# Optimization experiments

Hardware: AMD Instinct MI355X
Metric: run time of the kernel (lower is better)

The kernel has to match this reference:

```python
import jax, jax.numpy as jnp
import numpy as np

N = 8192
IN_F = 256
OUT_F = 256


def setup_inputs() -> dict:
    key = jax.random.key(0)
    k_v, k_adj, k1, k2, k3, kb = jax.random.split(key, 6)
    stdv = 1.0 / np.sqrt(OUT_F)
    V = jax.random.normal(k_v, (N, IN_F), dtype=jnp.float32)
    adj = jax.random.randint(k_adj, (N, N), 0, 4, dtype=jnp.int32)
    w1 = jax.random.uniform(k1, (IN_F, OUT_F), jnp.float32, -stdv, stdv)
    w2 = jax.random.uniform(k2, (IN_F, OUT_F), jnp.float32, -stdv, stdv)
    w3 = jax.random.uniform(k3, (IN_F, OUT_F), jnp.float32, -stdv, stdv)
    bias = jax.random.uniform(kb, (OUT_F,), jnp.float32, -stdv, stdv)
    return {"V": V, "adj": adj, "w1": w1, "w2": w2, "w3": w3, "bias": bias}


def reference(V, adj, w1, w2, w3, bias):
    # typed relational GCN: for each edge type k in {1,2,3},
    # aggregate (adj==k) @ (V @ wk), then sum and add bias
    o1 = jnp.matmul((adj == 1).astype(jnp.float32), jnp.matmul(V, w1))
    o2 = jnp.matmul((adj == 2).astype(jnp.float32), jnp.matmul(V, w2))
    o3 = jnp.matmul((adj == 3).astype(jnp.float32), jnp.matmul(V, w3))
    return o1 + o2 + o3 + bias
```

## Files before the change

kernel.cpp:

```cpp
#include <hip/hip_runtime.h>

typedef __attribute__((ext_vector_type(4))) float f32x4;
typedef __attribute__((ext_vector_type(16))) float f32x16;
typedef __attribute__((ext_vector_type(4))) unsigned short u16x4;
typedef __attribute__((ext_vector_type(4))) int i32x4;
typedef __attribute__((ext_vector_type(8))) __bf16 bf16x8;

union FragAB {
  u16x4 u[2];
  i32x4 v;
  bf16x8 f;
};

static __device__ __forceinline__ unsigned short f2bf(float x) {
  union { float f; unsigned u; } v;
  v.f = x;
  unsigned r = v.u + 0x7FFFu + ((v.u >> 16) & 1u);
  return (unsigned short)(r >> 16);
}

#define NN 8192

__global__ __launch_bounds__(256) void k_bias(const float* __restrict__ bias,
                                              float* __restrict__ out) {
  out[(size_t)blockIdx.x * 256 + threadIdx.x] = bias[threadIdx.x];
}

__global__ __launch_bounds__(256) void k_transform(
    const float* __restrict__ V, const float* __restrict__ w1,
    const float* __restrict__ w2, const float* __restrict__ w3,
    unsigned short* __restrict__ Bp) {
  int bx = blockIdx.x;
  int rb = bx & 63;
  int nb = bx >> 6;
  int nc0 = (nb & 3) * 64;
  int tid = threadIdx.x;
  int lane = tid & 63;
  int wv = tid >> 6;
  int wm = wv >> 1, wn = wv & 1;
  int q = lane >> 4, l16 = lane & 15;

  __shared__ unsigned short tA[128][36];
  __shared__ unsigned short tB[64][36];

  f32x4 acc[4][2];
#pragma unroll
  for (int i = 0; i < 4; i++)
#pragma unroll
    for (int j = 0; j < 2; j++) acc[i][j] = (f32x4)0.0f;

  for (int kk = 0; kk < 256; kk += 32) {
    {
      int r = tid >> 1, c0 = (tid & 1) * 16;
      const float* src = V + (size_t)(rb * 128 + r) * 256 + kk + c0;
      f32x4 f0 = *(const f32x4*)(src + 0);
      f32x4 f1 = *(const f32x4*)(src + 4);
      f32x4 f2 = *(const f32x4*)(src + 8);
      f32x4 f3 = *(const f32x4*)(src + 12);
      unsigned short* d = &tA[r][c0];
      d[0] = f2bf(f0.x);  d[1] = f2bf(f0.y);  d[2] = f2bf(f0.z);  d[3] = f2bf(f0.w);
      d[4] = f2bf(f1.x);  d[5] = f2bf(f1.y);  d[6] = f2bf(f1.z);  d[7] = f2bf(f1.w);
      d[8] = f2bf(f2.x);  d[9] = f2bf(f2.y);  d[10] = f2bf(f2.z); d[11] = f2bf(f2.w);
      d[12] = f2bf(f3.x); d[13] = f2bf(f3.y); d[14] = f2bf(f3.z); d[15] = f2bf(f3.w);
    }
    {
      int r = tid >> 3, cg = (tid & 7) * 8;
      size_t off = (size_t)(kk + r) * 256 + nc0 + cg;
      f32x4 g0, g1;
      if (nb < 4) {
        g0 = *(const f32x4*)(w1 + off);
        g1 = *(const f32x4*)(w1 + off + 4);
      } else if (nb < 8) {
        g0 = *(const f32x4*)(w2 + off);
        g1 = *(const f32x4*)(w2 + off + 4);
      } else {
        f32x4 a0 = *(const f32x4*)(w1 + off), a1 = *(const f32x4*)(w1 + off + 4);
        f32x4 b0 = *(const f32x4*)(w2 + off), b1 = *(const f32x4*)(w2 + off + 4);
        f32x4 d0 = *(const f32x4*)(w3 + off), d1 = *(const f32x4*)(w3 + off + 4);
        g0 = d0 - a0 - b0;
        g1 = d1 - a1 - b1;
      }
      tB[cg + 0][r] = f2bf(g0.x); tB[cg + 1][r] = f2bf(g0.y);
      tB[cg + 2][r] = f2bf(g0.z); tB[cg + 3][r] = f2bf(g0.w);
      tB[cg + 4][r] = f2bf(g1.x); tB[cg + 5][r] = f2bf(g1.y);
      tB[cg + 6][r] = f2bf(g1.z); tB[cg + 7][r] = f2bf(g1.w);
    }
    __syncthreads();
    FragAB af[4], bf[2];
#pragma unroll
    for (int mt = 0; mt < 4; mt++) {
      const unsigned short* p = &tA[wm * 64 + mt * 16 + l16][q * 8];
      af[mt].u[0] = *(const u16x4*)p;
      af[mt].u[1] = *(const u16x4*)(p + 4);
    }
#pragma unroll
    for (int nt = 0; nt < 2; nt++) {
      const unsigned short* p = &tB[wn * 32 + nt * 16 + l16][q * 8];
      bf[nt].u[0] = *(const u16x4*)p;
      bf[nt].u[1] = *(const u16x4*)(p + 4);
    }
#pragma unroll
    for (int mt = 0; mt < 4; mt++)
#pragma unroll
      for (int nt = 0; nt < 2; nt++)
        acc[mt][nt] = __builtin_amdgcn_mfma_f32_16x16x32_bf16(
            af[mt].f, bf[nt].f, acc[mt][nt], 0, 0, 0);
    __syncthreads();
  }
  int ty = nb >> 2;
#pragma unroll
  for (int mt = 0; mt < 4; mt++)
#pragma unroll
    for (int nt = 0; nt < 2; nt++) {
      int n = (nb & 3) * 64 + wn * 32 + nt * 16 + l16;
      int j0 = rb * 128 + wm * 64 + mt * 16 + q * 4;
      u16x4 hv;
      hv.x = f2bf(acc[mt][nt].x);
      hv.y = f2bf(acc[mt][nt].y);
      hv.z = f2bf(acc[mt][nt].z);
      hv.w = f2bf(acc[mt][nt].w);
      size_t idx = (size_t)ty * 2097152 + (size_t)(j0 >> 4) * 4096 + n * 16 + (j0 & 15);
      *(u16x4*)(Bp + idx) = hv;
    }
}

__global__ __launch_bounds__(256) void k_pack(const int* __restrict__ adj,
                                              unsigned* __restrict__ P) {
  int bx = blockIdx.x;
  int rowblk = bx >> 3, ks = bx & 7;
  int t = threadIdx.x;
  int r0 = rowblk * 32;
  __shared__ unsigned hal[32][129];

  int rl = t >> 7;
  int o = t & 127;
  const int* src0 = adj + (size_t)(r0 + rl) * NN + ks * 1024 + o * 8;
  i32x4 v0 = *(const i32x4*)src0;
  i32x4 v1 = *(const i32x4*)(src0 + 4);
  for (int p = 0; p < 16; p++) {
    i32x4 u0 = v0, u1 = v1;
    if (p < 15) {
      const int* s = src0 + (size_t)(p + 1) * 2 * NN;
      v0 = *(const i32x4*)s;
      v1 = *(const i32x4*)(s + 4);
    }
    unsigned b = (unsigned)(u0.x & 3) | ((unsigned)(u0.y & 3) << 2) |
                 ((unsigned)(u0.z & 3) << 4) | ((unsigned)(u0.w & 3) << 6) |
                 ((unsigned)(u1.x & 3) << 8) | ((unsigned)(u1.y & 3) << 10) |
                 ((unsigned)(u1.z & 3) << 12) | ((unsigned)(u1.w & 3) << 14);
    hal[p * 2 + rl][o] = b;
  }
  __syncthreads();
  for (int i = 0; i < 8; i++) {
    int oi = i * 256 + t;
    int row = oi & 31, sq = oi >> 5;
    int s = sq >> 1, q = sq & 1;
    unsigned lo = hal[row][s * 4 + q];
    unsigned hi = hal[row][s * 4 + 2 + q];
    P[((size_t)(ks * 32 + s) * 2 + q) * 8192 + r0 + row] = lo | (hi << 16);
  }
}

static __device__ __forceinline__ void expand2(unsigned bits, FragAB& fA,
                                               FragAB& fB) {
  unsigned short a[8], b[8];
#pragma unroll
  for (int e = 0; e < 8; e++) {
    a[e] = (bits & (1u << (2 * e))) ? 0x3F80 : 0;
    b[e] = (bits & (2u << (2 * e))) ? 0x3F80 : 0;
  }
  fA.u[0] = u16x4{a[0], a[1], a[2], a[3]};
  fA.u[1] = u16x4{a[4], a[5], a[6], a[7]};
  fB.u[0] = u16x4{b[0], b[1], b[2], b[3]};
  fB.u[1] = u16x4{b[4], b[5], b[6], b[7]};
}

__global__ __launch_bounds__(256, 2) void k_agg(const unsigned* __restrict__ P,
                                                const unsigned short* __restrict__ Bp,
                                                float* __restrict__ out) {
  int bx = blockIdx.x;
  int ks = bx & 7, rb = bx >> 3;
  int tid = threadIdx.x, lane = tid & 63;
  int wv = tid >> 6;
  int q = lane >> 5, l32 = lane & 31;

  f32x16 acc[4][2];
#pragma unroll
  for (int mt = 0; mt < 4; mt++) {
    acc[mt][0] = (f32x16)0.0f;
    acc[mt][1] = (f32x16)0.0f;
  }

  const unsigned* pp = P + ((size_t)ks * 64 + q) * 8192 + rb * 128 + l32;

  const unsigned short* bb[3][2];
#pragma unroll
  for (int ty = 0; ty < 3; ty++)
#pragma unroll
    for (int nt = 0; nt < 2; nt++) {
      int n = wv * 64 + nt * 32 + l32;
      bb[ty][nt] = Bp + (size_t)ty * 2097152 + (size_t)ks * 262144 + n * 16 + q * 8;
    }

  unsigned pk[4], npk[4];
#pragma unroll
  for (int mt = 0; mt < 4; mt++) pk[mt] = pp[mt * 32];

  for (int s = 0; s < 32; s++) {
    FragAB bv[2][3][2];
    size_t soff = (size_t)s * 8192;
#pragma unroll
    for (int kh = 0; kh < 2; kh++)
#pragma unroll
      for (int ty = 0; ty < 3; ty++)
#pragma unroll
        for (int nt = 0; nt < 2; nt++)
          bv[kh][ty][nt].v = *(const i32x4*)(bb[ty][nt] + soff + kh * 4096);
    if (s < 31) {
#pragma unroll
      for (int mt = 0; mt < 4; mt++)
        npk[mt] = pp[(size_t)(s + 1) * 16384 + mt * 32];
    }
#pragma unroll
    for (int mt = 0; mt < 4; mt++) {
#pragma unroll
      for (int kh = 0; kh < 2; kh++) {
        unsigned bits = (pk[mt] >> (kh * 16)) & 0xFFFFu;
        FragAB fA, fB, fC;
        expand2(bits, fA, fB);
        fC.v = fA.v & fB.v;
        acc[mt][0] = __builtin_amdgcn_mfma_f32_32x32x16_bf16(
            fA.f, bv[kh][0][0].f, acc[mt][0], 0, 0, 0);
        acc[mt][1] = __builtin_amdgcn_mfma_f32_32x32x16_bf16(
            fA.f, bv[kh][0][1].f, acc[mt][1], 0, 0, 0);
        acc[mt][0] = __builtin_amdgcn_mfma_f32_32x32x16_bf16(
            fB.f, bv[kh][1][0].f, acc[mt][0], 0, 0, 0);
        acc[mt][1] = __builtin_amdgcn_mfma_f32_32x32x16_bf16(
            fB.f, bv[kh][1][1].f, acc[mt][1], 0, 0, 0);
        acc[mt][0] = __builtin_amdgcn_mfma_f32_32x32x16_bf16(
            fC.f, bv[kh][2][0].f, acc[mt][0], 0, 0, 0);
        acc[mt][1] = __builtin_amdgcn_mfma_f32_32x32x16_bf16(
            fC.f, bv[kh][2][1].f, acc[mt][1], 0, 0, 0);
      }
    }
#pragma unroll
    for (int mt = 0; mt < 4; mt++) pk[mt] = npk[mt];
  }

#pragma unroll
  for (int mt = 0; mt < 4; mt++)
#pragma unroll
    for (int nt = 0; nt < 2; nt++) {
      int colbase = wv * 64 + nt * 32 + l32;
      int rowb = rb * 128 + mt * 32 + 4 * q;
#pragma unroll
      for (int r = 0; r < 16; r++) {
        int row = rowb + (r & 3) + 8 * (r >> 2);
        atomicAdd(out + (size_t)row * 256 + colbase, acc[mt][nt][r]);
      }
    }
}

extern "C" void kernel_launch(void* const* d_in, const int* in_sizes, int n_in,
                              void* d_out, int out_size, void* d_ws,
                              size_t ws_size, hipStream_t stream) {
  const float* V = (const float*)d_in[0];
  const int* adj = (const int*)d_in[1];
  const float* w1 = (const float*)d_in[2];
  const float* w2 = (const float*)d_in[3];
  const float* w3 = (const float*)d_in[4];
  const float* bias = (const float*)d_in[5];
  float* out = (float*)d_out;
  unsigned short* Bp = (unsigned short*)d_ws;
  unsigned* P = (unsigned*)((char*)d_ws + 12582912);

  k_bias<<<dim3(NN), dim3(256), 0, stream>>>(bias, out);
  k_pack<<<dim3(2048), dim3(256), 0, stream>>>(adj, P);
  k_transform<<<dim3(768), dim3(256), 0, stream>>>(V, w1, w2, w3, Bp);
  k_agg<<<dim3(512), dim3(256), 0, stream>>>(P, Bp, out);
}
```

Baseline: 541.2 us.

## Repack adjacency bits for multiply-based bf16 expansion and split aggregation tiles

The pack kernel now lays the two adjacency type bits out in separate nibbles, so the aggregation kernel can build bf16 one/zero fragments with a shift, mask and multiply by 0x3F80 instead of per-element selects. The aggregation kernel is retiled: each block covers half the output columns with a 2x2 wave grid and half the accumulators, doubling the grid to 1024 blocks and raising the occupancy hint to 3. This cuts the VALU work for fragment expansion and register pressure, but re-reads the packed adjacency twice and issues more atomics.

```diff
diff --git a/kernel.cpp b/kernel.cpp
--- a/kernel.cpp
+++ b/kernel.cpp
@@ -144,11 +144,16 @@
       v0 = *(const i32x4*)s;
       v1 = *(const i32x4*)(s + 4);
     }
-    unsigned b = (unsigned)(u0.x & 3) | ((unsigned)(u0.y & 3) << 2) |
-                 ((unsigned)(u0.z & 3) << 4) | ((unsigned)(u0.w & 3) << 6) |
-                 ((unsigned)(u1.x & 3) << 8) | ((unsigned)(u1.y & 3) << 10) |
-                 ((unsigned)(u1.z & 3) << 12) | ((unsigned)(u1.w & 3) << 14);
-    hal[p * 2 + rl][o] = b;
+    int cs[8] = {u0.x, u0.y, u0.z, u0.w, u1.x, u1.y, u1.z, u1.w};
+    unsigned code = 0;
+#pragma unroll
+    for (int j = 0; j < 4; j++) {
+      code |= (unsigned)(cs[2 * j] & 1) << j;
+      code |= (unsigned)((cs[2 * j] >> 1) & 1) << (8 + j);
+      code |= (unsigned)(cs[2 * j + 1] & 1) << (16 + j);
+      code |= (unsigned)((cs[2 * j + 1] >> 1) & 1) << (24 + j);
+    }
+    hal[p * 2 + rl][o] = code;
   }
   __syncthreads();
   for (int i = 0; i < 8; i++) {
@@ -157,54 +162,42 @@
     int s = sq >> 1, q = sq & 1;
     unsigned lo = hal[row][s * 4 + q];
     unsigned hi = hal[row][s * 4 + 2 + q];
-    P[((size_t)(ks * 32 + s) * 2 + q) * 8192 + r0 + row] = lo | (hi << 16);
-  }
-}
-
-static __device__ __forceinline__ void expand2(unsigned bits, FragAB& fA,
-                                               FragAB& fB) {
-  unsigned short a[8], b[8];
-#pragma unroll
-  for (int e = 0; e < 8; e++) {
-    a[e] = (bits & (1u << (2 * e))) ? 0x3F80 : 0;
-    b[e] = (bits & (2u << (2 * e))) ? 0x3F80 : 0;
-  }
-  fA.u[0] = u16x4{a[0], a[1], a[2], a[3]};
-  fA.u[1] = u16x4{a[4], a[5], a[6], a[7]};
-  fB.u[0] = u16x4{b[0], b[1], b[2], b[3]};
-  fB.u[1] = u16x4{b[4], b[5], b[6], b[7]};
-}
-
-__global__ __launch_bounds__(256, 2) void k_agg(const unsigned* __restrict__ P,
+    P[((size_t)(ks * 32 + s) * 2 + q) * 8192 + r0 + row] = lo | (hi << 4);
+  }
+}
+
+__global__ __launch_bounds__(256, 3) void k_agg(const unsigned* __restrict__ P,
                                                 const unsigned short* __restrict__ Bp,
                                                 float* __restrict__ out) {
   int bx = blockIdx.x;
-  int ks = bx & 7, rb = bx >> 3;
+  int ks = bx & 7;
+  int cb = (bx >> 3) & 1;
+  int rb = bx >> 4;
   int tid = threadIdx.x, lane = tid & 63;
   int wv = tid >> 6;
+  int wm = wv >> 1, wn = wv & 1;
   int q = lane >> 5, l32 = lane & 31;
 
-  f32x16 acc[4][2];
-#pragma unroll
-  for (int mt = 0; mt < 4; mt++) {
-    acc[mt][0] = (f32x16)0.0f;
-    acc[mt][1] = (f32x16)0.0f;
-  }
-
-  const unsigned* pp = P + ((size_t)ks * 64 + q) * 8192 + rb * 128 + l32;
+  f32x16 acc[2][2];
+  acc[0][0] = (f32x16)0.0f;
+  acc[0][1] = (f32x16)0.0f;
+  acc[1][0] = (f32x16)0.0f;
+  acc[1][1] = (f32x16)0.0f;
+
+  const unsigned* pp = P + ((size_t)ks * 64 + q) * 8192 + rb * 128 + wm * 64 + l32;
 
   const unsigned short* bb[3][2];
 #pragma unroll
   for (int ty = 0; ty < 3; ty++)
 #pragma unroll
     for (int nt = 0; nt < 2; nt++) {
-      int n = wv * 64 + nt * 32 + l32;
+      int n = cb * 128 + wn * 64 + nt * 32 + l32;
       bb[ty][nt] = Bp + (size_t)ty * 2097152 + (size_t)ks * 262144 + n * 16 + q * 8;
     }
 
-  unsigned pk[4], npk[4];
-#pragma unroll
-  for (int mt = 0; mt < 4; mt++) pk[mt] = pp[mt * 32];
+  unsigned pk[2], npk[2] = {0, 0};
+  pk[0] = pp[0];
+  pk[1] = pp[32];
 
   for (int s = 0; s < 32; s++) {
     FragAB bv[2][3][2];
@@ -217,18 +210,25 @@
         for (int nt = 0; nt < 2; nt++)
           bv[kh][ty][nt].v = *(const i32x4*)(bb[ty][nt] + soff + kh * 4096);
     if (s < 31) {
-#pragma unroll
-      for (int mt = 0; mt < 4; mt++)
-        npk[mt] = pp[(size_t)(s + 1) * 16384 + mt * 32];
-    }
-#pragma unroll
-    for (int mt = 0; mt < 4; mt++) {
+      npk[0] = pp[(size_t)(s + 1) * 16384];
+      npk[1] = pp[(size_t)(s + 1) * 16384 + 32];
+    }
+#pragma unroll
+    for (int mt = 0; mt < 2; mt++) {
+      unsigned w = pk[mt];
 #pragma unroll
       for (int kh = 0; kh < 2; kh++) {
-        unsigned bits = (pk[mt] >> (kh * 16)) & 0xFFFFu;
         FragAB fA, fB, fC;
-        expand2(bits, fA, fB);
-        fC.v = fA.v & fB.v;
+#pragma unroll
+        for (int j = 0; j < 4; j++) {
+          unsigned a = (w >> (4 * kh + j)) & 0x10001u;
+          unsigned b = (w >> (4 * kh + j + 8)) & 0x10001u;
+          unsigned fa = a * 0x3F80u;
+          unsigned fb = b * 0x3F80u;
+          fA.v[j] = (int)fa;
+          fB.v[j] = (int)fb;
+          fC.v[j] = (int)(fa & fb);
+        }
         acc[mt][0] = __builtin_amdgcn_mfma_f32_32x32x16_bf16(
             fA.f, bv[kh][0][0].f, acc[mt][0], 0, 0, 0);
         acc[mt][1] = __builtin_amdgcn_mfma_f32_32x32x16_bf16(
@@ -243,16 +243,16 @@
             fC.f, bv[kh][2][1].f, acc[mt][1], 0, 0, 0);
       }
     }
-#pragma unroll
-    for (int mt = 0; mt < 4; mt++) pk[mt] = npk[mt];
-  }
-
-#pragma unroll
-  for (int mt = 0; mt < 4; mt++)
-#pragma unroll
-    for (int nt = 0; nt < 2; nt++) {
-      int colbase = wv * 64 + nt * 32 + l32;
-      int rowb = rb * 128 + mt * 32 + 4 * q;
+    pk[0] = npk[0];
+    pk[1] = npk[1];
+  }
+
+#pragma unroll
+  for (int mt = 0; mt < 2; mt++)
+#pragma unroll
+    for (int nt = 0; nt < 2; nt++) {
+      int colbase = cb * 128 + wn * 64 + nt * 32 + l32;
+      int rowb = rb * 128 + wm * 64 + mt * 32 + 4 * q;
 #pragma unroll
       for (int r = 0; r < 16; r++) {
         int row = rowb + (r & 3) + 8 * (r >> 2);
@@ -277,5 +277,5 @@
   k_bias<<<dim3(NN), dim3(256), 0, stream>>>(bias, out);
   k_pack<<<dim3(2048), dim3(256), 0, stream>>>(adj, P);
   k_transform<<<dim3(768), dim3(256), 0, stream>>>(V, w1, w2, w3, Bp);
-  k_agg<<<dim3(512), dim3(256), 0, stream>>>(P, Bp, out);
-}
+  k_agg<<<dim3(1024), dim3(256), 0, stream>>>(P, Bp, out);
+}
```

After: 505.3 us. 1.07x faster.
